# Kernel optimization log

Measured on AMD Instinct MI355X. Metric: run time of the kernel, lower is better.

The kernel has to match this reference:

```python
import jax, jax.numpy as jnp
import numpy as np

WIN = 7
N = WIN * WIN  # 49 tokens per window
C = 384
H = 12
HD = C // H
B_ = 4096
NW = 64  # number of distinct window masks; must divide B_


def _relative_position_index(wh=WIN, ww=WIN):
    coords = np.stack(np.meshgrid(np.arange(wh), np.arange(ww), indexing='ij'))  # [2,wh,ww]
    cf = coords.reshape(2, -1)
    rel = cf[:, :, None] - cf[:, None, :]               # [2,N,N]
    rel = rel.transpose(1, 2, 0).astype(np.int32)       # [N,N,2]
    rel[:, :, 0] += wh - 1
    rel[:, :, 1] += ww - 1
    rel[:, :, 0] *= 2 * ww - 1
    return jnp.asarray(rel.sum(-1))                     # [N,N] int32


def setup_inputs() -> dict:
    key = jax.random.key(0)
    ks = jax.random.split(key, 8)
    std = 0.02
    return {
        'x': jax.random.normal(ks[0], (B_, N, C), jnp.float32),
        'mask': jnp.zeros((NW, N, N), jnp.float32),  # 0/-inf mask; zeros here
        'qkv_w': jax.random.normal(ks[1], (3 * C, C), jnp.float32) * std,
        'qkv_b': jnp.zeros((3 * C,), jnp.float32),
        'rpb_table': jax.random.normal(ks[2], ((2 * WIN - 1) ** 2, H), jnp.float32) * std,
        'proj_l_w': jax.random.normal(ks[3], (H, H), jnp.float32) * std,
        'proj_l_b': jnp.zeros((H,), jnp.float32),
        'proj_w_w': jax.random.normal(ks[4], (H, H), jnp.float32) * std,
        'proj_w_b': jnp.zeros((H,), jnp.float32),
        'proj_weight': jax.random.normal(ks[5], (C, C), jnp.float32) * std,
        'proj_bias': jnp.zeros((C,), jnp.float32),
        'rel_index': _relative_position_index(),
    }


def reference(x, mask, qkv_w, qkv_b, rpb_table, proj_l_w, proj_l_b,
              proj_w_w, proj_w_b, proj_weight, proj_bias, rel_index):
    B, n, c = x.shape
    scale = HD ** (-0.5)
    qkv = x @ qkv_w.T + qkv_b                     # [B,N,3C]
    q_out, k_out, v_out = jnp.split(qkv, 3, axis=-1)  # each [B,N,C]
    qkv5 = qkv.reshape(B, n, 3, H, HD)
    q = qkv5[:, :, 0].transpose(0, 2, 1, 3)       # [B,H,N,hd]
    k = qkv5[:, :, 1].transpose(0, 2, 1, 3)
    v = qkv5[:, :, 2].transpose(0, 2, 1, 3)
    attn = jnp.einsum('bhnd,bhmd->bhnm', q * scale, k)   # [B,H,N,N]
    bias = rpb_table[rel_index]                   # [N,N,H]
    attn = attn + bias.transpose(2, 0, 1)[None]
    # proj_l: linear mixing across heads (Linear acts on last dim after permute)
    attn = jnp.einsum('bhnm,gh->bgnm', attn, proj_l_w) + proj_l_b[None, :, None, None]
    nW = mask.shape[0]
    attn = attn.reshape(B // nW, nW, H, n, n) + mask[None, :, None]
    attn = attn.reshape(B, H, n, n)
    attn = jax.nn.softmax(attn, axis=-1)
    # proj_w: head mixing after softmax
    attn = jnp.einsum('bhnm,gh->bgnm', attn, proj_w_w) + proj_w_b[None, :, None, None]
    out = jnp.einsum('bhnm,bhmd->bnhd', attn, v).reshape(B, n, c)
    out = out @ proj_weight.T + proj_bias
    return (out, (q_out, k_out, v_out))
```

## Files before the change

### kernel.cpp

```cpp
#include <hip/hip_runtime.h>
#include <hip/hip_bf16.h>

#define TOK 49
#define NPT 2401
#define CDIM 384
#define NH 12
#define HDIM 32
#define NWIN 64
#define BTOT 4096
#define OUTSZ (BTOT * TOK * CDIM)
#define L2E 1.4426950408889634f

typedef __attribute__((ext_vector_type(8))) short bf16x8;
typedef __attribute__((ext_vector_type(4))) float f32x4;
typedef unsigned int uint32;
typedef unsigned short ushort_t;

__device__ inline ushort_t f2bf(float f) {
  uint32 u = __float_as_uint(f);
  u += 0x7FFF + ((u >> 16) & 1);
  return (ushort_t)(u >> 16);
}
__device__ inline uint32 pk2(float a, float b) {
  union { __hip_bfloat162 h; uint32 u; } x;
  x.h = __float22bfloat162_rn(float2{a, b});
  return x.u;
}
__device__ inline float bf2f(uint32 u) { return __uint_as_float((u & 0xffffu) << 16); }
__device__ inline bf16x8 pack8(float4 a, float4 b) {
  union { __hip_bfloat162 h[4]; bf16x8 v; } u;
  u.h[0] = __float22bfloat162_rn(float2{a.x, a.y});
  u.h[1] = __float22bfloat162_rn(float2{a.z, a.w});
  u.h[2] = __float22bfloat162_rn(float2{b.x, b.y});
  u.h[3] = __float22bfloat162_rn(float2{b.z, b.w});
  return u.v;
}
__device__ inline bf16x8 pack8f(const float* f) {
  union { __hip_bfloat162 h[4]; bf16x8 v; } u;
#pragma unroll
  for (int i = 0; i < 4; ++i) u.h[i] = __float22bfloat162_rn(float2{f[2*i], f[2*i+1]});
  return u.v;
}

__global__ void k_cvt(const float* __restrict__ src, ushort_t* __restrict__ dst, int n8) {
  int i = blockIdx.x * 256 + threadIdx.x;
  if (i >= n8) return;
  const float4* s = (const float4*)(src + (size_t)i * 8);
  float4 a = s[0], b = s[1];
  uint4 o;
  o.x = (uint32)f2bf(a.x) | ((uint32)f2bf(a.y) << 16);
  o.y = (uint32)f2bf(a.z) | ((uint32)f2bf(a.w) << 16);
  o.z = (uint32)f2bf(b.x) | ((uint32)f2bf(b.y) << 16);
  o.w = (uint32)f2bf(b.z) | ((uint32)f2bf(b.w) << 16);
  *(uint4*)(dst + (size_t)i * 8) = o;
}

__global__ void k_bias2(const float* __restrict__ rpb, const float* __restrict__ plw,
                        const float* __restrict__ plb, const int* __restrict__ relidx,
                        ushort_t* __restrict__ bmf) {
  int i = blockIdx.x * 256 + threadIdx.x;
  if (i >= NPT * 12) return;
  int p = i / 12, g = i - (i / 12) * 12;
  int rid = relidx[p];
  float s = plb[g];
#pragma unroll
  for (int h = 0; h < NH; ++h) s = fmaf(plw[g * NH + h], rpb[rid * NH + h], s);
  bmf[i] = f2bf(s * L2E);
}

__launch_bounds__(256)
__global__ void k_qkv_mfma(const ushort_t* __restrict__ Xb, const ushort_t* __restrict__ Wb,
                           const float* __restrict__ Bq, float* __restrict__ qslab) {
  __shared__ ushort_t As[128 * 32];
  __shared__ ushort_t Bs[128 * 32];
  const int bid = blockIdx.x;
  const int sw = (bid & 7) * 1764 + (bid >> 3);
  const int bx = sw / 9;
  const int by = sw - bx * 9;
  const int tid = threadIdx.x;
  const int l = tid & 63;
  const int wv = tid >> 6;
  const int wr = wv >> 1, wc = wv & 1;
  const int row0 = bx * 128;
  const int col0 = by * 128;

  f32x4 acc[4][4];
#pragma unroll
  for (int i = 0; i < 4; ++i)
#pragma unroll
    for (int j = 0; j < 4; ++j)
#pragma unroll
      for (int e = 0; e < 4; ++e) acc[i][j][e] = 0.f;

  for (int kb = 0; kb < CDIM; kb += 32) {
#pragma unroll
    for (int i = 0; i < 2; ++i) {
      int cid = tid + i * 256;
      int r = cid >> 2, c = cid & 3;
      uint4 v = *(const uint4*)&Xb[(size_t)(row0 + r) * CDIM + kb + c * 8];
      *(uint4*)&As[r * 32 + c * 8] = v;
      uint4 w = *(const uint4*)&Wb[(size_t)(col0 + r) * CDIM + kb + c * 8];
      *(uint4*)&Bs[r * 32 + c * 8] = w;
    }
    __syncthreads();
    bf16x8 af[4], bfr[4];
#pragma unroll
    for (int mt = 0; mt < 4; ++mt)
      af[mt] = *(const bf16x8*)&As[(wr * 64 + mt * 16 + (l & 15)) * 32 + (l >> 4) * 8];
#pragma unroll
    for (int nt = 0; nt < 4; ++nt)
      bfr[nt] = *(const bf16x8*)&Bs[(wc * 64 + nt * 16 + (l & 15)) * 32 + (l >> 4) * 8];
#pragma unroll
    for (int mt = 0; mt < 4; ++mt)
#pragma unroll
      for (int nt = 0; nt < 4; ++nt)
        acc[mt][nt] = __builtin_amdgcn_mfma_f32_16x16x32_bf16(af[mt], bfr[nt], acc[mt][nt], 0, 0, 0);
    __syncthreads();
  }

  const int slab = by / 3;
  const int cslab0 = col0 - slab * CDIM;
  float* dst = qslab + (size_t)slab * OUTSZ;
#pragma unroll
  for (int nt = 0; nt < 4; ++nt) {
    int colg = col0 + wc * 64 + nt * 16 + (l & 15);
    int colo = cslab0 + wc * 64 + nt * 16 + (l & 15);
    float bv = Bq[colg];
#pragma unroll
    for (int mt = 0; mt < 4; ++mt) {
      int rbase = row0 + wr * 64 + mt * 16 + (l >> 4) * 4;
#pragma unroll
      for (int j = 0; j < 4; ++j)
        dst[(size_t)(rbase + j) * CDIM + colo] = acc[mt][nt][j] + bv;
    }
  }
}

__launch_bounds__(1024, 8)
__global__ void k_attn9(const float* __restrict__ qslab, const float* __restrict__ kslab,
                        const float* __restrict__ vslab, const float* __restrict__ mask,
                        const ushort_t* __restrict__ bmf, const float* __restrict__ plw,
                        const float* __restrict__ pww, const float* __restrict__ pwb,
                        float* __restrict__ xout) {
  __shared__ __align__(16) ushort_t SA[19976];
  __shared__ __align__(16) ushort_t PP[12 * 1400 + 416];

  const int tid = threadIdx.x;
  const int b  = blockIdx.x >> 1;
  const int bh = blockIdx.x & 1;
  const int n0 = bh * 25;
  const int NR = bh ? 24 : 25;
  const size_t base = (size_t)b * TOK * CDIM;
  const int l = tid & 63, l15 = l & 15, l16 = l >> 4;
  const int wv = tid >> 6;
  const float SCL = 0.17677669529663687f * L2E;

  for (int p = tid; p < 1240; p += 1024) *(uint2*)&SA[p * 16 + 12] = uint2{0u, 0u};
  if (tid < 580) *(uint32*)&SA[18816 + tid * 2] = 0u;
  if (tid < 208) *(uint32*)&PP[12 * 1400 + tid * 2] = 0u;

  {
    const int art = wv >> 3;
    const int act = (wv >> 1) & 3;
    const int ah0 = (wv & 1) * 6;
    const int nrow = art * 16 + l15;
    const int mrow = act * 16 + l15;
    const bool qv = nrow < NR;
    const bool kv = mrow < TOK;
#pragma unroll
    for (int hp = 0; hp < 3; ++hp) {
      f32x4 s2[2];
#pragma unroll
      for (int hh = 0; hh < 2; ++hh) {
        int h = ah0 + hp * 2 + hh;
        bf16x8 af = {0,0,0,0,0,0,0,0}, bf = {0,0,0,0,0,0,0,0};
        if (qv) {
          const float4* qp = (const float4*)(qslab + base + (size_t)(n0 + nrow) * CDIM + h * HDIM + l16 * 8);
          af = pack8(qp[0], qp[1]);
        }
        if (kv) {
          const float4* kp = (const float4*)(kslab + base + (size_t)mrow * CDIM + h * HDIM + l16 * 8);
          bf = pack8(kp[0], kp[1]);
        }
        f32x4 z = {0.f, 0.f, 0.f, 0.f};
        s2[hh] = __builtin_amdgcn_mfma_f32_16x16x32_bf16(af, bf, z, 0, 0, 0);
      }
#pragma unroll
      for (int j = 0; j < 4; ++j) {
        int nj = art * 16 + l16 * 4 + j;
        if (nj < NR && kv)
          *(uint32*)&SA[(nj * 49 + mrow) * 16 + ah0 + hp * 2] = pk2(s2[0][j], s2[1][j]);
      }
    }
  }
  __syncthreads();

  {
    const float* maskw = mask + (size_t)(b & (NWIN - 1)) * NPT;
    float apf[8], bpf[8];
#pragma unroll
    for (int j = 0; j < 8; ++j) {
      int kj = l16 * 8 + j;
      apf[j] = (l15 < NH && kj < NH) ? plw[l15 * NH + kj] * SCL : 0.f;
      bpf[j] = (l15 < NH && kj < NH) ? pww[l15 * NH + kj] : 0.f;
    }
    const bf16x8 aplw = pack8f(apf);
    const bf16x8 bpww = pack8f(bpf);
    const float pwbv = (l15 < NH) ? pwb[l15] : 0.f;

    for (int nl = wv; nl < NR; nl += 1024 / 64) {
      const int pb0 = nl * 49;
      float ev[4][4];
      float rs[4] = {0.f, 0.f, 0.f, 0.f};
#pragma unroll
      for (int mc = 0; mc < 4; ++mc) {
        int m = mc * 16 + l15;
        int pl = pb0 + m;
        bf16x8 sf = {0,0,0,0,0,0,0,0};
        if (l16 < 2) sf = *(const bf16x8*)&SA[pl * 16 + l16 * 8];
        int pg = pl + n0 * 49; if (pg > 2400) pg = 2400;
        uint2 bmu = *(const uint2*)&bmf[pg * 12 + l16 * 4];
        float mk = maskw[pg] * L2E;
        f32x4 cini = {bf2f(bmu.x) + mk, bf2f(bmu.x >> 16) + mk,
                      bf2f(bmu.y) + mk, bf2f(bmu.y >> 16) + mk};
        f32x4 o = __builtin_amdgcn_mfma_f32_16x16x32_bf16(aplw, sf, cini, 0, 0, 0);
        bool okm = (m < TOK);
#pragma unroll
        for (int j = 0; j < 4; ++j) {
          int g = l16 * 4 + j;
          float e = (okm && g < NH) ? exp2f(o[j]) : 0.f;
          ev[mc][j] = e;
          rs[j] += e;
        }
      }
#pragma unroll
      for (int d = 1; d < 16; d <<= 1)
#pragma unroll
        for (int j = 0; j < 4; ++j) rs[j] += __shfl_xor(rs[j], d, 64);
      float inv[4];
#pragma unroll
      for (int j = 0; j < 4; ++j) inv[j] = (rs[j] > 0.f) ? 1.f / rs[j] : 0.f;

#pragma unroll
      for (int mc = 0; mc < 4; ++mc) {
        int m = mc * 16 + l15;
        if (m < TOK) {
          uint2 w;
          w.x = pk2(ev[mc][0] * inv[0], ev[mc][1] * inv[1]);
          w.y = pk2(ev[mc][2] * inv[2], ev[mc][3] * inv[3]);
          *(uint2*)&SA[(pb0 + m) * 16 + l16 * 4] = w;
        }
      }
#pragma unroll
      for (int mc = 0; mc < 4; ++mc) {
        bf16x8 pf8 = {0,0,0,0,0,0,0,0};
        if (l16 < 2) pf8 = *(const bf16x8*)&SA[(pb0 + mc * 16 + l15) * 16 + l16 * 8];
        f32x4 cd = {pwbv, pwbv, pwbv, pwbv};
        f32x4 o = __builtin_amdgcn_mfma_f32_16x16x32_bf16(pf8, bpww, cd, 0, 0, 0);
        int m0 = mc * 16 + l16 * 4;
        if (l15 < NH && m0 < 56) {
          float z0 = (m0     < TOK) ? o[0] : 0.f;
          float z1 = (m0 + 1 < TOK) ? o[1] : 0.f;
          float z2 = (m0 + 2 < TOK) ? o[2] : 0.f;
          float z3 = (m0 + 3 < TOK) ? o[3] : 0.f;
          uint2 w;
          w.x = pk2(z0, z1);
          w.y = pk2(z2, z3);
          *(uint2*)&PP[l15 * 1400 + nl * 56 + m0] = w;
        }
      }
    }
  }
  __syncthreads();

  {
    ushort_t* Vt = SA;
    for (int i = tid; i < CDIM * 13; i += 1024) {
      int mq = i / CDIM, c = i - mq * CDIM;
      int m = mq * 4;
      float f0 = (m     < TOK) ? vslab[base + (size_t)(m    ) * CDIM + c] : 0.f;
      float f1 = (m + 1 < TOK) ? vslab[base + (size_t)(m + 1) * CDIM + c] : 0.f;
      float f2 = (m + 2 < TOK) ? vslab[base + (size_t)(m + 2) * CDIM + c] : 0.f;
      float f3 = (m + 3 < TOK) ? vslab[base + (size_t)(m + 3) * CDIM + c] : 0.f;
      uint2 u;
      u.x = pk2(f0, f1);
      u.y = pk2(f2, f3);
      *(uint2*)&Vt[c * 52 + mq * 4] = u;
    }
  }
  __syncthreads();

  {
    const ushort_t* Vt = SA;
    const int ert = wv >> 3;
    const int edt = (wv >> 2) & 1;
    const int egq = wv & 3;
#pragma unroll
    for (int gi = 0; gi < 3; ++gi) {
      int g = egq * 3 + gi;
      int col = g * HDIM + edt * 16 + l15;
      f32x4 acc = {0.f, 0.f, 0.f, 0.f};
#pragma unroll
      for (int ks = 0; ks < 2; ++ks) {
        bf16x8 pa8 = {0,0,0,0,0,0,0,0};
        bf16x8 vb8 = {0,0,0,0,0,0,0,0};
        if (!(ks == 1 && l16 == 3)) {
          pa8 = *(const bf16x8*)&PP[g * 1400 + (ert * 16 + l15) * 56 + ks * 32 + l16 * 8];
          uint2 lo = *(const uint2*)&Vt[col * 52 + ks * 32 + l16 * 8];
          uint2 hi = *(const uint2*)&Vt[col * 52 + ks * 32 + l16 * 8 + 4];
          union { uint32 u[4]; bf16x8 v; } uv;
          uv.u[0] = lo.x; uv.u[1] = lo.y; uv.u[2] = hi.x; uv.u[3] = hi.y;
          vb8 = uv.v;
        }
        acc = __builtin_amdgcn_mfma_f32_16x16x32_bf16(pa8, vb8, acc, 0, 0, 0);
      }
#pragma unroll
      for (int j = 0; j < 4; ++j) {
        int nlo = ert * 16 + l16 * 4 + j;
        if (nlo < NR)
          xout[base + (size_t)(n0 + nlo) * CDIM + col] = acc[j];
      }
    }
  }
}

__launch_bounds__(512, 4)
__global__ void k_proj3(float* __restrict__ Y, const float* __restrict__ W,
                        const float* __restrict__ Bv) {
  __shared__ __align__(16) ushort_t Asb[64 * 392];
  __shared__ __align__(16) ushort_t Bsb[384 * 40];
  const int tid = threadIdx.x;
  const int l = tid & 63, l15 = l & 15, l16 = l >> 4;
  const int wv = tid >> 6;
  const int wr = wv >> 2;
  const int wc = wv & 3;
  const int row0 = blockIdx.x * 64;

#pragma unroll
  for (int i = 0; i < 6; ++i) {
    int cid = tid + i * 512;
    int r = cid / 48, c8 = cid - (cid / 48) * 48;
    const float4* s = (const float4*)&Y[(size_t)(row0 + r) * CDIM + c8 * 8];
    float4 a = s[0], b = s[1];
    uint4 o;
    o.x = pk2(a.x, a.y); o.y = pk2(a.z, a.w);
    o.z = pk2(b.x, b.y); o.w = pk2(b.z, b.w);
    *(uint4*)&Asb[r * 392 + c8 * 8] = o;
  }

  f32x4 acc[2][6];
#pragma unroll
  for (int i = 0; i < 2; ++i)
#pragma unroll
    for (int j = 0; j < 6; ++j)
#pragma unroll
      for (int e = 0; e < 4; ++e) acc[i][j][e] = 0.f;

  for (int kb = 0; kb < 12; ++kb) {
    __syncthreads();
#pragma unroll
    for (int i = 0; i < 3; ++i) {
      int cid = tid + i * 512;
      int col = cid >> 2, k8 = cid & 3;
      const float4* s = (const float4*)&W[(size_t)col * CDIM + kb * 32 + k8 * 8];
      float4 a = s[0], b = s[1];
      uint4 o;
      o.x = pk2(a.x, a.y); o.y = pk2(a.z, a.w);
      o.z = pk2(b.x, b.y); o.w = pk2(b.z, b.w);
      *(uint4*)&Bsb[col * 40 + k8 * 8] = o;
    }
    __syncthreads();
    bf16x8 af[2], bfr[6];
#pragma unroll
    for (int mt = 0; mt < 2; ++mt)
      af[mt] = *(const bf16x8*)&Asb[(wr * 32 + mt * 16 + l15) * 392 + kb * 32 + l16 * 8];
#pragma unroll
    for (int nt = 0; nt < 6; ++nt)
      bfr[nt] = *(const bf16x8*)&Bsb[(wc * 96 + nt * 16 + l15) * 40 + l16 * 8];
#pragma unroll
    for (int mt = 0; mt < 2; ++mt)
#pragma unroll
      for (int nt = 0; nt < 6; ++nt)
        acc[mt][nt] = __builtin_amdgcn_mfma_f32_16x16x32_bf16(af[mt], bfr[nt], acc[mt][nt], 0, 0, 0);
  }

#pragma unroll
  for (int nt = 0; nt < 6; ++nt) {
    int col = wc * 96 + nt * 16 + l15;
    float bv = Bv[col];
#pragma unroll
    for (int mt = 0; mt < 2; ++mt) {
      int rbase = row0 + wr * 32 + mt * 16 + l16 * 4;
#pragma unroll
      for (int j = 0; j < 4; ++j)
        Y[(size_t)(rbase + j) * CDIM + col] = acc[mt][nt][j] + bv;
    }
  }
}

extern "C" void kernel_launch(void* const* d_in, const int* in_sizes, int n_in,
                              void* d_out, int out_size, void* d_ws, size_t ws_size,
                              hipStream_t stream) {
  const float* x      = (const float*)d_in[0];
  const float* mask   = (const float*)d_in[1];
  const float* qkv_w  = (const float*)d_in[2];
  const float* qkv_b  = (const float*)d_in[3];
  const float* rpb    = (const float*)d_in[4];
  const float* plw    = (const float*)d_in[5];
  const float* plb    = (const float*)d_in[6];
  const float* pww    = (const float*)d_in[7];
  const float* pwb    = (const float*)d_in[8];
  const float* projw  = (const float*)d_in[9];
  const float* projb  = (const float*)d_in[10];
  const int*   relidx = (const int*)d_in[11];

  float* out   = (float*)d_out;
  float* qslab = out + (size_t)OUTSZ;
  float* kslab = out + 2 * (size_t)OUTSZ;
  float* vslab = out + 3 * (size_t)OUTSZ;

  ushort_t* Xb  = (ushort_t*)out;
  ushort_t* Wb  = (ushort_t*)(out + 70000000);
  ushort_t* bmf = (ushort_t*)d_ws;

  k_cvt<<<(OUTSZ / 8 + 255) / 256, 256, 0, stream>>>(x, Xb, OUTSZ / 8);
  k_cvt<<<(3 * CDIM * CDIM / 8 + 255) / 256, 256, 0, stream>>>(qkv_w, Wb, 3 * CDIM * CDIM / 8);
  k_bias2<<<(NPT * 12 + 255) / 256, 256, 0, stream>>>(rpb, plw, plb, relidx, bmf);

  k_qkv_mfma<<<(BTOT * TOK / 128) * 9, 256, 0, stream>>>(Xb, Wb, qkv_b, qslab);

  k_attn9<<<BTOT * 2, 1024, 0, stream>>>(qslab, kslab, vslab, mask, bmf,
                                         plw, pww, pwb, out);

  k_proj3<<<BTOT * TOK / 64, 512, 0, stream>>>(out, projw, projb);
}
```

Measured before the change: 1.330 ms.

## Double K-tile depth with XOR-swizzled LDS in QKV GEMM; fold mask into bias table

The QKV GEMM now stages 64-wide K slices per iteration instead of 32. That halves the number of barrier pairs, and an XOR swizzle on the LDS index is meant to avoid bank conflicts on the fragment reads. Separately, when the workspace is large enough, a new kernel precomputes a per-window bias table that already includes the mask. The attention kernel then skips the separate mask load and add. The cost is doubled shared memory per GEMM block, which may lower occupancy, and a 64x larger bias table read from memory.

```diff
diff --git a/kernel.cpp b/kernel.cpp
--- a/kernel.cpp
+++ b/kernel.cpp
@@ -68,17 +68,32 @@
   bmf[i] = f2bf(s * L2E);
 }
 
+__global__ void k_bias3(const float* __restrict__ rpb, const float* __restrict__ plw,
+                        const float* __restrict__ plb, const int* __restrict__ relidx,
+                        const float* __restrict__ mask, ushort_t* __restrict__ bmfw) {
+  int i = blockIdx.x * 256 + threadIdx.x;
+  if (i >= NWIN * NPT * 12) return;
+  int w = i / (NPT * 12);
+  int rem = i - w * (NPT * 12);
+  int p = rem / 12, g = rem - (rem / 12) * 12;
+  int rid = relidx[p];
+  float s = plb[g];
+#pragma unroll
+  for (int h = 0; h < NH; ++h) s = fmaf(plw[g * NH + h], rpb[rid * NH + h], s);
+  bmfw[i] = f2bf((s + mask[w * NPT + p]) * L2E);
+}
+
 __launch_bounds__(256)
 __global__ void k_qkv_mfma(const ushort_t* __restrict__ Xb, const ushort_t* __restrict__ Wb,
                            const float* __restrict__ Bq, float* __restrict__ qslab) {
-  __shared__ ushort_t As[128 * 32];
-  __shared__ ushort_t Bs[128 * 32];
+  __shared__ __align__(16) ushort_t As[128 * 64];
+  __shared__ __align__(16) ushort_t Bs[128 * 64];
   const int bid = blockIdx.x;
   const int sw = (bid & 7) * 1764 + (bid >> 3);
   const int bx = sw / 9;
   const int by = sw - bx * 9;
   const int tid = threadIdx.x;
-  const int l = tid & 63;
+  const int l = tid & 63, l15 = l & 15, l16 = l >> 4;
   const int wv = tid >> 6;
   const int wr = wv >> 1, wc = wv & 1;
   const int row0 = bx * 128;
@@ -92,29 +107,39 @@
 #pragma unroll
       for (int e = 0; e < 4; ++e) acc[i][j][e] = 0.f;
 
-  for (int kb = 0; kb < CDIM; kb += 32) {
-#pragma unroll
-    for (int i = 0; i < 2; ++i) {
-      int cid = tid + i * 256;
-      int r = cid >> 2, c = cid & 3;
-      uint4 v = *(const uint4*)&Xb[(size_t)(row0 + r) * CDIM + kb + c * 8];
-      *(uint4*)&As[r * 32 + c * 8] = v;
-      uint4 w = *(const uint4*)&Wb[(size_t)(col0 + r) * CDIM + kb + c * 8];
-      *(uint4*)&Bs[r * 32 + c * 8] = w;
+  const int sr = tid >> 3, sc = tid & 7;
+  const int sidx = (sr * 64 + sc * 8) ^ ((sr & 7) << 3);
+
+  for (int kb = 0; kb < CDIM; kb += 64) {
+#pragma unroll
+    for (int i = 0; i < 4; ++i) {
+      int r = sr + i * 32;
+      int idx = (sidx + i * 32 * 64) ^ 0;
+      uint4 v = *(const uint4*)&Xb[(size_t)(row0 + r) * CDIM + kb + sc * 8];
+      *(uint4*)&As[idx] = v;
+      uint4 w = *(const uint4*)&Wb[(size_t)(col0 + r) * CDIM + kb + sc * 8];
+      *(uint4*)&Bs[idx] = w;
     }
     __syncthreads();
-    bf16x8 af[4], bfr[4];
-#pragma unroll
-    for (int mt = 0; mt < 4; ++mt)
-      af[mt] = *(const bf16x8*)&As[(wr * 64 + mt * 16 + (l & 15)) * 32 + (l >> 4) * 8];
-#pragma unroll
-    for (int nt = 0; nt < 4; ++nt)
-      bfr[nt] = *(const bf16x8*)&Bs[(wc * 64 + nt * 16 + (l & 15)) * 32 + (l >> 4) * 8];
-#pragma unroll
-    for (int mt = 0; mt < 4; ++mt)
-#pragma unroll
-      for (int nt = 0; nt < 4; ++nt)
-        acc[mt][nt] = __builtin_amdgcn_mfma_f32_16x16x32_bf16(af[mt], bfr[nt], acc[mt][nt], 0, 0, 0);
+#pragma unroll
+    for (int ks = 0; ks < 2; ++ks) {
+      bf16x8 af[4], bfr[4];
+#pragma unroll
+      for (int mt = 0; mt < 4; ++mt) {
+        int row = wr * 64 + mt * 16 + l15;
+        af[mt] = *(const bf16x8*)&As[(row * 64 + ks * 32 + l16 * 8) ^ ((row & 7) << 3)];
+      }
+#pragma unroll
+      for (int nt = 0; nt < 4; ++nt) {
+        int row = wc * 64 + nt * 16 + l15;
+        bfr[nt] = *(const bf16x8*)&Bs[(row * 64 + ks * 32 + l16 * 8) ^ ((row & 7) << 3)];
+      }
+#pragma unroll
+      for (int mt = 0; mt < 4; ++mt)
+#pragma unroll
+        for (int nt = 0; nt < 4; ++nt)
+          acc[mt][nt] = __builtin_amdgcn_mfma_f32_16x16x32_bf16(af[mt], bfr[nt], acc[mt][nt], 0, 0, 0);
+    }
     __syncthreads();
   }
 
@@ -123,12 +148,12 @@
   float* dst = qslab + (size_t)slab * OUTSZ;
 #pragma unroll
   for (int nt = 0; nt < 4; ++nt) {
-    int colg = col0 + wc * 64 + nt * 16 + (l & 15);
-    int colo = cslab0 + wc * 64 + nt * 16 + (l & 15);
+    int colg = col0 + wc * 64 + nt * 16 + l15;
+    int colo = cslab0 + wc * 64 + nt * 16 + l15;
     float bv = Bq[colg];
 #pragma unroll
     for (int mt = 0; mt < 4; ++mt) {
-      int rbase = row0 + wr * 64 + mt * 16 + (l >> 4) * 4;
+      int rbase = row0 + wr * 64 + mt * 16 + l16 * 4;
 #pragma unroll
       for (int j = 0; j < 4; ++j)
         dst[(size_t)(rbase + j) * CDIM + colo] = acc[mt][nt][j] + bv;
@@ -139,9 +164,9 @@
 __launch_bounds__(1024, 8)
 __global__ void k_attn9(const float* __restrict__ qslab, const float* __restrict__ kslab,
                         const float* __restrict__ vslab, const float* __restrict__ mask,
-                        const ushort_t* __restrict__ bmf, const float* __restrict__ plw,
-                        const float* __restrict__ pww, const float* __restrict__ pwb,
-                        float* __restrict__ xout) {
+                        const ushort_t* __restrict__ bmf, int wstride,
+                        const float* __restrict__ plw, const float* __restrict__ pww,
+                        const float* __restrict__ pwb, float* __restrict__ xout) {
   __shared__ __align__(16) ushort_t SA[19976];
   __shared__ __align__(16) ushort_t PP[12 * 1400 + 416];
 
@@ -196,7 +221,8 @@
   __syncthreads();
 
   {
-    const float* maskw = mask + (size_t)(b & (NWIN - 1)) * NPT;
+    const float* maskw = mask ? (mask + (size_t)(b & (NWIN - 1)) * NPT) : nullptr;
+    const ushort_t* bmw = bmf + (size_t)(b & (NWIN - 1)) * wstride;
     float apf[8], bpf[8];
 #pragma unroll
     for (int j = 0; j < 8; ++j) {
@@ -208,7 +234,7 @@
     const bf16x8 bpww = pack8f(bpf);
     const float pwbv = (l15 < NH) ? pwb[l15] : 0.f;
 
-    for (int nl = wv; nl < NR; nl += 1024 / 64) {
+    for (int nl = wv; nl < NR; nl += 16) {
       const int pb0 = nl * 49;
       float ev[4][4];
       float rs[4] = {0.f, 0.f, 0.f, 0.f};
@@ -219,10 +245,12 @@
         bf16x8 sf = {0,0,0,0,0,0,0,0};
         if (l16 < 2) sf = *(const bf16x8*)&SA[pl * 16 + l16 * 8];
         int pg = pl + n0 * 49; if (pg > 2400) pg = 2400;
-        uint2 bmu = *(const uint2*)&bmf[pg * 12 + l16 * 4];
-        float mk = maskw[pg] * L2E;
-        f32x4 cini = {bf2f(bmu.x) + mk, bf2f(bmu.x >> 16) + mk,
-                      bf2f(bmu.y) + mk, bf2f(bmu.y >> 16) + mk};
+        uint2 bmu = *(const uint2*)&bmw[pg * 12 + l16 * 4];
+        f32x4 cini = {bf2f(bmu.x), bf2f(bmu.x >> 16), bf2f(bmu.y), bf2f(bmu.y >> 16)};
+        if (maskw) {
+          float mk = maskw[pg] * L2E;
+          cini[0] += mk; cini[1] += mk; cini[2] += mk; cini[3] += mk;
+        }
         f32x4 o = __builtin_amdgcn_mfma_f32_16x16x32_bf16(aplw, sf, cini, 0, 0, 0);
         bool okm = (m < TOK);
 #pragma unroll
@@ -425,11 +453,19 @@
 
   k_cvt<<<(OUTSZ / 8 + 255) / 256, 256, 0, stream>>>(x, Xb, OUTSZ / 8);
   k_cvt<<<(3 * CDIM * CDIM / 8 + 255) / 256, 256, 0, stream>>>(qkv_w, Wb, 3 * CDIM * CDIM / 8);
-  k_bias2<<<(NPT * 12 + 255) / 256, 256, 0, stream>>>(rpb, plw, plb, relidx, bmf);
+
+  const size_t need_ws = (size_t)NWIN * NPT * 12 * sizeof(ushort_t);
+  const bool folded = (ws_size >= need_ws);
+  if (folded)
+    k_bias3<<<(NWIN * NPT * 12 + 255) / 256, 256, 0, stream>>>(rpb, plw, plb, relidx, mask, bmf);
+  else
+    k_bias2<<<(NPT * 12 + 255) / 256, 256, 0, stream>>>(rpb, plw, plb, relidx, bmf);
 
   k_qkv_mfma<<<(BTOT * TOK / 128) * 9, 256, 0, stream>>>(Xb, Wb, qkv_b, qslab);
 
-  k_attn9<<<BTOT * 2, 1024, 0, stream>>>(qslab, kslab, vslab, mask, bmf,
+  k_attn9<<<BTOT * 2, 1024, 0, stream>>>(qslab, kslab, vslab,
+                                         folded ? nullptr : mask, bmf,
+                                         folded ? NPT * 12 : 0,
                                          plw, pww, pwb, out);
 
   k_proj3<<<BTOT * TOK / 64, 512, 0, stream>>>(out, projw, projb);
```

Result: no change. 1.319 ms (-0.8%).
